# Kernel tuning notes

Hardware: AMD Instinct MI355X
Metric: run time of the kernel (lower is better)

## Reference

```python
import jax, jax.numpy as jnp
import numpy as np

EPS = 1e-3  # nn.LayerNorm(eps=0.001)
PADDING = 0.0


def setup_inputs() -> dict:
    key = jax.random.key(0)
    k1, k2, k3, k4 = jax.random.split(key, 4)
    N, M, K3, C_IN, C_OUT, B = 200000, 40000, 27, 64, 128, 4
    features = jax.random.normal(k1, (N, C_IN), dtype=jnp.float32)
    center_coors = jax.random.normal(k2, (M, 3), dtype=jnp.float32)
    voxel_idx = jax.random.randint(k3, (M, K3), 0, N, dtype=jnp.int64)
    num_list = jnp.full((B,), M // B, dtype=jnp.int32)
    W = jax.random.normal(k4, (K3 * C_IN, C_OUT), dtype=jnp.float32) * 1e-4
    gamma = jnp.ones((C_OUT,), dtype=jnp.float32)
    beta = jnp.zeros((C_OUT,), dtype=jnp.float32)
    return {
        "features": features,
        "center_coors": center_coors,
        "voxel_idx": voxel_idx,
        "num_list": num_list,
        "W": W,
        "gamma": gamma,
        "beta": beta,
        "num_keypoints": 2048,
    }


def _block(features, voxel_idx, W, gamma, beta):
    M, K3 = voxel_idx.shape
    C_in = features.shape[1]
    # voxel neighbor gather; negative idx -> padding value
    gathered = features[jnp.clip(voxel_idx, 0, features.shape[0] - 1)]  # [M, K3, C_in]
    gathered = jnp.where(voxel_idx[..., None] < 0, PADDING, gathered)
    flat = gathered.reshape(M, K3 * C_in)
    out = flat @ W  # [M, C_out]
    # LayerNorm over channel dim (per-batch loop in torch is mathematically
    # identical to a single row-wise LayerNorm)
    mu = jnp.mean(out, axis=-1, keepdims=True)
    var = jnp.mean(jnp.square(out - mu), axis=-1, keepdims=True)
    out = (out - mu) / jnp.sqrt(var + EPS) * gamma + beta
    return jax.nn.relu(out)


def _resample(out_features, center_coors, num_list, num_keypoints):
    B = num_list.shape[0]
    K = num_keypoints
    accum = jnp.cumsum(num_list)
    offsets = jnp.concatenate([jnp.zeros((1,), accum.dtype), accum[:-1]])  # [B]
    j = jnp.arange(K, dtype=jnp.int32)  # [K]
    end = jnp.minimum(num_list, jnp.int32(K))  # [B]
    valid = j[None, :] < end[:, None]  # [B, K]
    src = jnp.clip(offsets[:, None] + j[None, :], 0, out_features.shape[0] - 1)  # [B, K]
    res_feat = jnp.where(valid[..., None], out_features[src], 0.0)  # [B, K, C]
    res_xyz = jnp.where(valid[..., None], center_coors[src], 0.0)  # [B, K, 3]
    # replicate original quirk: segments 0..B-2 get batch index 1..B-1, last stays 0
    bid = jnp.arange(B, dtype=jnp.float32)
    col0 = jnp.where(bid < B - 1, bid + 1.0, 0.0)  # [B]
    col0 = jnp.broadcast_to(col0[:, None, None], (B, K, 1))
    res_coor = jnp.concatenate([col0, res_xyz], axis=-1)  # [B, K, 4]
    C = out_features.shape[1]
    return res_feat.reshape(B * K, C), res_coor.reshape(B * K, 4)


def reference(features, center_coors, voxel_idx, num_list, W, gamma, beta, num_keypoints):
    out = _block(features, voxel_idx, W, gamma, beta)
    point_features, point_coords = _resample(out, center_coors, num_list, num_keypoints)
    return point_features, point_coords
```

## Files before the change

### kernel.cpp

```cpp
#include <hip/hip_runtime.h>
#include <hip/hip_bf16.h>
#include <stdint.h>
#include <stddef.h>

#define TM 16
#define CIN 64
#define NK3 27
#define NK3P 28
#define COUT 128
#define EPS_LN 1e-3f
#define KCH  (NK3 * CIN / 32)
#define KCHP (NK3P * CIN / 32)
#define NT   (COUT / 16)
#define NPAIR (NK3P / 2)
#define PK_BYTES (NT * KCHP * 64 * 8 * 2)

typedef __attribute__((ext_vector_type(8))) short   short8;
typedef __attribute__((ext_vector_type(4))) float   floatx4;
typedef __attribute__((ext_vector_type(4))) unsigned short ushort4v;

__device__ __forceinline__ unsigned short f2b(float f) {
    union { float f; unsigned int i; } v;
    v.f = f;
    unsigned int i = v.i;
    return (unsigned short)((i + 0x7fffu + ((i >> 16) & 1u)) >> 16);
}

__global__ __launch_bounds__(256) void pack_w(const float* __restrict__ Wm,
                                              const int* __restrict__ voxel_idx,
                                              const int* __restrict__ num_list,
                                              int Bc,
                                              unsigned short* __restrict__ pk,
                                              int* __restrict__ flags) {
    const int t = threadIdx.x;
    if (blockIdx.x == 0 && t < 64) {
        int wv = voxel_idx[2 * t + 1];
        unsigned long long nz = __ballot(wv != 0);
        if (t == 0) {
            int f = (nz == 0ULL) ? 1 : 0;
            bool n64 = false;
            if (Bc >= 2) {
                n64 = (num_list[1] == 0) && (num_list[0] != 0);
                if (Bc >= 4) n64 = n64 && (num_list[3] == 0);
            }
            if (n64) f |= 2;
            flags[0] = f;
        }
    }
    int slot = blockIdx.x * 256 + t;
    int l  = slot & 63;
    int kk = (slot >> 6) % KCHP;
    int nt = slot / (64 * KCHP);
    short8 v = {0, 0, 0, 0, 0, 0, 0, 0};
    if (kk < KCH) {
        int q = l >> 4, n = l & 15;
        const float* src = Wm + (size_t)(kk * 32 + q * 8) * COUT + nt * 16 + n;
        #pragma unroll
        for (int j = 0; j < 8; ++j)
            v[j] = (short)f2b(src[(size_t)j * COUT]);
    }
    *(short8*)(pk + (size_t)slot * 8) = v;
}

__global__ __launch_bounds__(512) void dpc_mfma(
    const float* __restrict__ features,
    const float* __restrict__ center,
    const int* __restrict__ voxel_idx,
    const int* __restrict__ num_list,
    const unsigned short* __restrict__ pk,
    const int* __restrict__ flags,
    const float* __restrict__ gamma_,
    const float* __restrict__ beta_,
    float* __restrict__ out_feat,
    float* __restrict__ out_coor,
    int N, int M, int B, int K, int Rtot)
{
    __shared__ int s_vid[TM][NK3P];
    __shared__ int s_src[TM];
    __shared__ int s_valid[TM];
    __shared__ __align__(16) unsigned short s_a[3][2048];
    __shared__ float s_c[TM][COUT + 4];

    const int t  = threadIdx.x;
    const int R0 = blockIdx.x * TM;

    const int fl = flags[0];
    const bool vidx64 = (fl & 1) != 0;
    const bool nl64   = (fl & 2) != 0;

    if (t < TM) {
        int r = R0 + t;
        int src = 0, valid = 0;
        if (r < Rtot) {
            int b = r / K;
            int j = r - b * K;
            int offs = 0, nlb = 0;
            for (int i = 0; i < B; ++i) {
                int v = nl64 ? num_list[2 * i] : num_list[i];
                if (i < b) offs += v;
                if (i == b) nlb = v;
            }
            int end = nlb < K ? nlb : K;
            valid = (j < end) ? 1 : 0;
            src = offs + j;
            if (src < 0) src = 0;
            if (src > M - 1) src = M - 1;
        }
        s_src[t] = src;
        s_valid[t] = valid;
    }
    __syncthreads();

    if (t < TM * 4) {
        int i = t >> 2, comp = t & 3;
        int r = R0 + i;
        if (r < Rtot) {
            float val;
            if (comp == 0) {
                int b = r / K;
                val = (b < B - 1) ? (float)(b + 1) : 0.0f;
            } else {
                val = s_valid[i] ? center[(size_t)s_src[i] * 3 + comp - 1] : 0.0f;
            }
            out_coor[(size_t)r * 4 + comp] = val;
        }
    }

    for (int lin = t; lin < TM * NK3P; lin += 512) {
        int i = lin / NK3P;
        int k = lin - i * NK3P;
        int v = -1;
        if (k < NK3) {
            size_t e = (size_t)s_src[i] * NK3 + k;
            v = vidx64 ? voxel_idx[2 * e] : voxel_idx[e];
        }
        s_vid[i][k] = v;
    }
    __syncthreads();

    const int sub = t >> 8;
    const int rem = t & 255;
    const int m   = rem >> 4;
    const int c0  = (rem & 15) * 4;
    const int chunk = c0 >> 5;
    const int q4    = (c0 & 31) >> 3;
    const int j0    = c0 & 7;
    const int aoff  = sub * 1024 + chunk * 512 + (q4 * 16 + m) * 8 + j0;

    auto gatherPair = [&](int p) -> float4 {
        int idx = s_vid[m][2 * p + sub];
        float4 r = make_float4(0.f, 0.f, 0.f, 0.f);
        if (idx >= 0) {
            if (idx > N - 1) idx = N - 1;
            r = *(const float4*)(features + (size_t)idx * CIN + c0);
        }
        return r;
    };
    auto stash = [&](int buf, float4 v) {
        ushort4v u;
        u[0] = f2b(v.x); u[1] = f2b(v.y); u[2] = f2b(v.z); u[3] = f2b(v.w);
        *(ushort4v*)&s_a[buf][aoff] = u;
    };

    const int w    = t >> 6;
    const int lane = t & 63;
    auto loadB = [&](int kk) -> short8 {
        return *(const short8*)(pk + ((size_t)(w * KCHP + kk) * 64 + lane) * 8);
    };

    floatx4 acc = {0.f, 0.f, 0.f, 0.f};

    stash(0, gatherPair(0));
    float4 cA = gatherPair(1);
    short8 bb0 = loadB(0), bb1 = loadB(1), bb2 = loadB(2), bb3 = loadB(3);
    __syncthreads();

    for (int p = 0; p < NPAIR; ++p) {
        const bool hasC = (p + 1 < NPAIR);
        const bool hasN = (p + 2 < NPAIR);

        float4 nA;
        if (hasN) nA = gatherPair(p + 2);
        short8 nb0, nb1, nb2, nb3;
        if (hasC) {
            const int kk = 4 * (p + 1);
            nb0 = loadB(kk); nb1 = loadB(kk + 1); nb2 = loadB(kk + 2); nb3 = loadB(kk + 3);
        }

        const int buf = p % 3;
        const short8 a0 = *(const short8*)&s_a[buf][       lane * 8];
        const short8 a1 = *(const short8*)&s_a[buf][ 512 + lane * 8];
        const short8 a2 = *(const short8*)&s_a[buf][1024 + lane * 8];
        const short8 a3 = *(const short8*)&s_a[buf][1536 + lane * 8];

        acc = __builtin_amdgcn_mfma_f32_16x16x32_bf16(a0, bb0, acc, 0, 0, 0);
        acc = __builtin_amdgcn_mfma_f32_16x16x32_bf16(a1, bb1, acc, 0, 0, 0);
        acc = __builtin_amdgcn_mfma_f32_16x16x32_bf16(a2, bb2, acc, 0, 0, 0);
        acc = __builtin_amdgcn_mfma_f32_16x16x32_bf16(a3, bb3, acc, 0, 0, 0);

        if (hasC) stash((p + 1) % 3, cA);
        __syncthreads();
        if (hasC) { bb0 = nb0; bb1 = nb1; bb2 = nb2; bb3 = nb3; }
        if (hasN) cA = nA;
    }

    {
        const int cq = lane >> 4, n = lane & 15;
        #pragma unroll
        for (int reg = 0; reg < 4; ++reg)
            s_c[cq * 4 + reg][w * 16 + n] = acc[reg];
    }
    __syncthreads();

    const int c2 = lane * 2;
    const float g0  = gamma_[c2];
    const float g1  = gamma_[c2 + 1];
    const float be0 = beta_[c2];
    const float be1 = beta_[c2 + 1];

    #pragma unroll
    for (int i = 0; i < 2; ++i) {
        int row = w * 2 + i;
        float a0 = s_c[row][c2];
        float a1 = s_c[row][c2 + 1];
        float s  = a0 + a1;
        float ss = a0 * a0 + a1 * a1;
        #pragma unroll
        for (int mm = 1; mm < 64; mm <<= 1) {
            s  += __shfl_xor(s,  mm, 64);
            ss += __shfl_xor(ss, mm, 64);
        }
        float mu   = s * (1.0f / COUT);
        float var  = ss * (1.0f / COUT) - mu * mu;
        float rstd = rsqrtf(var + EPS_LN);
        float v0 = (a0 - mu) * rstd * g0 + be0;
        float v1 = (a1 - mu) * rstd * g1 + be1;
        v0 = fmaxf(v0, 0.f);
        v1 = fmaxf(v1, 0.f);
        if (!s_valid[row]) { v0 = 0.f; v1 = 0.f; }
        int r = R0 + row;
        if (r < Rtot) {
            out_feat[(size_t)r * COUT + c2]     = v0;
            out_feat[(size_t)r * COUT + c2 + 1] = v1;
        }
    }
}

extern "C" void kernel_launch(void* const* d_in, const int* in_sizes, int n_in,
                              void* d_out, int out_size, void* d_ws, size_t ws_size,
                              hipStream_t stream) {
    const float* features = (const float*)d_in[0];
    const float* center   = (const float*)d_in[1];
    const int*   vidx     = (const int*)d_in[2];
    const int*   num_list = (const int*)d_in[3];
    const float* Wm       = (const float*)d_in[4];
    const float* gamma_   = (const float*)d_in[5];
    const float* beta_    = (const float*)d_in[6];

    const int B    = in_sizes[3];
    const int Cout = in_sizes[5];
    const int M    = in_sizes[1] / 3;
    const int K3v  = in_sizes[2] / M;
    const int Cin  = (in_sizes[4] / Cout) / K3v;
    const int N    = in_sizes[0] / Cin;
    const int Rtot = out_size / (Cout + 4);
    const int K    = Rtot / B;

    float* out_feat = (float*)d_out;
    float* out_coor = out_feat + (size_t)Rtot * Cout;

    unsigned short* pk = (unsigned short*)d_ws;
    int* flags = (int*)((char*)d_ws + PK_BYTES);

    const int pack_grid = (NT * KCHP * 64) / 256;
    pack_w<<<dim3(pack_grid), dim3(256), 0, stream>>>(Wm, vidx, num_list, B, pk, flags);

    const int tiles = (Rtot + TM - 1) / TM;
    dpc_mfma<<<dim3(tiles), dim3(512), 0, stream>>>(
        features, center, vidx, num_list, pk, flags, gamma_, beta_,
        out_feat, out_coor, N, M, B, K, Rtot);
}
```

Measured before the change: 111.3 us.

## Process four kernel offsets per barrier and pack weights through shared memory

The main loop now handles slabs of four neighbor offsets (8 MFMAs) per __syncthreads instead of pairs (4 MFMAs), which halves the barrier count and doubles the gather batch in flight per thread. The A staging buffer doubles in size. The weight packing kernel is restructured so each block stages a 32-row slice of W in shared memory with coalesced float4 loads, replacing strided global reads. In exchange the kernel uses more LDS and more registers for the extra B fragments and prefetches, which may lower occupancy.

```diff
diff --git a/kernel.cpp b/kernel.cpp
--- a/kernel.cpp
+++ b/kernel.cpp
@@ -12,7 +12,7 @@
 #define KCH  (NK3 * CIN / 32)
 #define KCHP (NK3P * CIN / 32)
 #define NT   (COUT / 16)
-#define NPAIR (NK3P / 2)
+#define NSLAB (NK3P / 4)
 #define PK_BYTES (NT * KCHP * 64 * 8 * 2)
 
 typedef __attribute__((ext_vector_type(8))) short   short8;
@@ -32,8 +32,11 @@
                                               int Bc,
                                               unsigned short* __restrict__ pk,
                                               int* __restrict__ flags) {
-    const int t = threadIdx.x;
-    if (blockIdx.x == 0 && t < 64) {
+    __shared__ float s_w[32][COUT + 1];
+    const int t  = threadIdx.x;
+    const int kk = blockIdx.x;
+
+    if (kk == 0 && t < 64) {
         int wv = voxel_idx[2 * t + 1];
         unsigned long long nz = __ballot(wv != 0);
         if (t == 0) {
@@ -47,19 +50,34 @@
             flags[0] = f;
         }
     }
-    int slot = blockIdx.x * 256 + t;
-    int l  = slot & 63;
-    int kk = (slot >> 6) % KCHP;
-    int nt = slot / (64 * KCHP);
-    short8 v = {0, 0, 0, 0, 0, 0, 0, 0};
+
     if (kk < KCH) {
-        int q = l >> 4, n = l & 15;
-        const float* src = Wm + (size_t)(kk * 32 + q * 8) * COUT + nt * 16 + n;
         #pragma unroll
-        for (int j = 0; j < 8; ++j)
-            v[j] = (short)f2b(src[(size_t)j * COUT]);
-    }
-    *(short8*)(pk + (size_t)slot * 8) = v;
+        for (int i = 0; i < 4; ++i) {
+            int s   = t + i * 256;
+            int row = s >> 5;
+            int c4  = (s & 31) * 4;
+            float4 v = *(const float4*)(Wm + (size_t)(kk * 32 + row) * COUT + c4);
+            s_w[row][c4 + 0] = v.x; s_w[row][c4 + 1] = v.y;
+            s_w[row][c4 + 2] = v.z; s_w[row][c4 + 3] = v.w;
+        }
+    }
+    __syncthreads();
+
+    #pragma unroll
+    for (int i = 0; i < 2; ++i) {
+        int slot = t + i * 256;
+        int l  = slot & 63;
+        int nt = slot >> 6;
+        int q  = l >> 4, n = l & 15;
+        short8 v = {0, 0, 0, 0, 0, 0, 0, 0};
+        if (kk < KCH) {
+            #pragma unroll
+            for (int j = 0; j < 8; ++j)
+                v[j] = (short)f2b(s_w[q * 8 + j][nt * 16 + n]);
+        }
+        *(short8*)(pk + ((size_t)(nt * KCHP + kk) * 64 + l) * 8) = v;
+    }
 }
 
 __global__ __launch_bounds__(512) void dpc_mfma(
@@ -78,7 +96,7 @@
     __shared__ int s_vid[TM][NK3P];
     __shared__ int s_src[TM];
     __shared__ int s_valid[TM];
-    __shared__ __align__(16) unsigned short s_a[3][2048];
+    __shared__ __align__(16) unsigned short s_a[3][4096];
     __shared__ float s_c[TM][COUT + 4];
 
     const int t  = threadIdx.x;
@@ -138,17 +156,17 @@
     }
     __syncthreads();
 
-    const int sub = t >> 8;
-    const int rem = t & 255;
-    const int m   = rem >> 4;
-    const int c0  = (rem & 15) * 4;
+    const int sub0  = t >> 8;
+    const int rem   = t & 255;
+    const int m     = rem >> 4;
+    const int c0    = (rem & 15) * 4;
     const int chunk = c0 >> 5;
     const int q4    = (c0 & 31) >> 3;
     const int j0    = c0 & 7;
-    const int aoff  = sub * 1024 + chunk * 512 + (q4 * 16 + m) * 8 + j0;
-
-    auto gatherPair = [&](int p) -> float4 {
-        int idx = s_vid[m][2 * p + sub];
+    const int aoffA = sub0 * 1024 + chunk * 512 + (q4 * 16 + m) * 8 + j0;
+
+    auto gatherOne = [&](int kc) -> float4 {
+        int idx = s_vid[m][kc];
         float4 r = make_float4(0.f, 0.f, 0.f, 0.f);
         if (idx >= 0) {
             if (idx > N - 1) idx = N - 1;
@@ -156,10 +174,12 @@
         }
         return r;
     };
-    auto stash = [&](int buf, float4 v) {
+    auto stash = [&](int buf, float4 vA, float4 vB) {
         ushort4v u;
-        u[0] = f2b(v.x); u[1] = f2b(v.y); u[2] = f2b(v.z); u[3] = f2b(v.w);
-        *(ushort4v*)&s_a[buf][aoff] = u;
+        u[0] = f2b(vA.x); u[1] = f2b(vA.y); u[2] = f2b(vA.z); u[3] = f2b(vA.w);
+        *(ushort4v*)&s_a[buf][aoffA] = u;
+        u[0] = f2b(vB.x); u[1] = f2b(vB.y); u[2] = f2b(vB.z); u[3] = f2b(vB.w);
+        *(ushort4v*)&s_a[buf][aoffA + 2048] = u;
     };
 
     const int w    = t >> 6;
@@ -170,38 +190,53 @@
 
     floatx4 acc = {0.f, 0.f, 0.f, 0.f};
 
-    stash(0, gatherPair(0));
-    float4 cA = gatherPair(1);
+    float4 p0  = gatherOne(sub0),     p1  = gatherOne(sub0 + 2);
+    float4 cA0 = gatherOne(4 + sub0), cA1 = gatherOne(4 + sub0 + 2);
     short8 bb0 = loadB(0), bb1 = loadB(1), bb2 = loadB(2), bb3 = loadB(3);
-    __syncthreads();
-
-    for (int p = 0; p < NPAIR; ++p) {
-        const bool hasC = (p + 1 < NPAIR);
-        const bool hasN = (p + 2 < NPAIR);
-
-        float4 nA;
-        if (hasN) nA = gatherPair(p + 2);
+    stash(0, p0, p1);
+    __syncthreads();
+
+    for (int q = 0; q < NSLAB; ++q) {
+        const bool hasC = (q + 1 < NSLAB);
+        const bool hasN = (q + 2 < NSLAB);
+
+        float4 nA0, nA1;
+        if (hasN) {
+            nA0 = gatherOne(4 * (q + 2) + sub0);
+            nA1 = gatherOne(4 * (q + 2) + sub0 + 2);
+        }
+        const int kb = 8 * q;
+        short8 bb4 = loadB(kb + 4), bb5 = loadB(kb + 5),
+               bb6 = loadB(kb + 6), bb7 = loadB(kb + 7);
         short8 nb0, nb1, nb2, nb3;
         if (hasC) {
-            const int kk = 4 * (p + 1);
-            nb0 = loadB(kk); nb1 = loadB(kk + 1); nb2 = loadB(kk + 2); nb3 = loadB(kk + 3);
-        }
-
-        const int buf = p % 3;
-        const short8 a0 = *(const short8*)&s_a[buf][       lane * 8];
-        const short8 a1 = *(const short8*)&s_a[buf][ 512 + lane * 8];
-        const short8 a2 = *(const short8*)&s_a[buf][1024 + lane * 8];
-        const short8 a3 = *(const short8*)&s_a[buf][1536 + lane * 8];
-
+            nb0 = loadB(kb + 8);  nb1 = loadB(kb + 9);
+            nb2 = loadB(kb + 10); nb3 = loadB(kb + 11);
+        }
+
+        const int buf = q % 3;
+        const unsigned short* sa = &s_a[buf][0];
+        const short8 a0 = *(const short8*)&sa[       lane * 8];
+        const short8 a1 = *(const short8*)&sa[ 512 + lane * 8];
+        const short8 a2 = *(const short8*)&sa[1024 + lane * 8];
+        const short8 a3 = *(const short8*)&sa[1536 + lane * 8];
         acc = __builtin_amdgcn_mfma_f32_16x16x32_bf16(a0, bb0, acc, 0, 0, 0);
         acc = __builtin_amdgcn_mfma_f32_16x16x32_bf16(a1, bb1, acc, 0, 0, 0);
         acc = __builtin_amdgcn_mfma_f32_16x16x32_bf16(a2, bb2, acc, 0, 0, 0);
         acc = __builtin_amdgcn_mfma_f32_16x16x32_bf16(a3, bb3, acc, 0, 0, 0);
-
-        if (hasC) stash((p + 1) % 3, cA);
+        const short8 a4 = *(const short8*)&sa[2048 + lane * 8];
+        const short8 a5 = *(const short8*)&sa[2560 + lane * 8];
+        const short8 a6 = *(const short8*)&sa[3072 + lane * 8];
+        const short8 a7 = *(const short8*)&sa[3584 + lane * 8];
+        acc = __builtin_amdgcn_mfma_f32_16x16x32_bf16(a4, bb4, acc, 0, 0, 0);
+        acc = __builtin_amdgcn_mfma_f32_16x16x32_bf16(a5, bb5, acc, 0, 0, 0);
+        acc = __builtin_amdgcn_mfma_f32_16x16x32_bf16(a6, bb6, acc, 0, 0, 0);
+        acc = __builtin_amdgcn_mfma_f32_16x16x32_bf16(a7, bb7, acc, 0, 0, 0);
+
+        if (hasC) stash((q + 1) % 3, cA0, cA1);
         __syncthreads();
         if (hasC) { bb0 = nb0; bb1 = nb1; bb2 = nb2; bb3 = nb3; }
-        if (hasN) cA = nA;
+        if (hasN) { cA0 = nA0; cA1 = nA1; }
     }
 
     {
@@ -272,8 +307,7 @@
     unsigned short* pk = (unsigned short*)d_ws;
     int* flags = (int*)((char*)d_ws + PK_BYTES);
 
-    const int pack_grid = (NT * KCHP * 64) / 256;
-    pack_w<<<dim3(pack_grid), dim3(256), 0, stream>>>(Wm, vidx, num_list, B, pk, flags);
+    pack_w<<<dim3(KCHP), dim3(256), 0, stream>>>(Wm, vidx, num_list, B, pk, flags);
 
     const int tiles = (Rtot + TM - 1) / TM;
     dpc_mfma<<<dim3(tiles), dim3(512), 0, stream>>>(
```

After: 111.5 us. Within noise of the previous version (+0.2%).
